# Optimization experiments

Hardware: AMD Instinct MI355X
Metric: run time of the kernel (lower is better)

## Reference

```python
import jax, jax.numpy as jnp
import numpy as np

OUT = 16          # output_size
SCALE = 1.0 / 16.0  # 1/featmap_stride
GRID = 2          # sampling_ratio


def setup_inputs() -> dict:
    key = jax.random.key(0)
    k1, k2, k3 = jax.random.split(key, 3)
    N, C, T, H, W, K = 2, 256, 16, 56, 56, 5
    feat = jax.random.normal(k1, (N, C, T, H, W), jnp.float32)
    img = H * 16.0  # 896 px input image
    xy = jax.random.uniform(k2, (N, K, 2), minval=0.0, maxval=img - 300.0)
    wh = jax.random.uniform(k3, (N, K, 2), minval=32.0, maxval=290.0)
    boxes = jnp.concatenate([xy, xy + wh], axis=-1)  # valid xyxy boxes
    rois = jnp.concatenate([jnp.zeros((N, K, 1)), boxes], axis=-1).astype(jnp.float32)
    entity_mask = jnp.ones((N, 1, K, T), dtype=bool)  # unused by forward (as in original)
    return {"feat": feat, "rois": rois, "entity_mask": entity_mask}


def _roi_align_single(feat_n, boxes):
    """RoIAlign (aligned=True, avg pool, fixed sampling grid) for one clip.

    feat_n: (C, T, H, W) -- applied to every frame t at once.
    boxes:  (K, 4) xyxy in input-image coordinates.
    returns (T, K, C, OUT, OUT)
    """
    C, T, H, W = feat_n.shape
    K = boxes.shape[0]
    b = boxes * SCALE - 0.5  # aligned=True offset
    x1, y1, x2, y2 = b[:, 0], b[:, 1], b[:, 2], b[:, 3]
    bin_w = (x2 - x1) / OUT
    bin_h = (y2 - y1) / OUT
    g = (jnp.arange(GRID, dtype=feat_n.dtype) + 0.5) / GRID
    p = jnp.arange(OUT, dtype=feat_n.dtype)
    # sample coords per roi/bin/grid-point: (K, OUT, GRID)
    xs = x1[:, None, None] + (p[None, :, None] + g[None, None, :]) * bin_w[:, None, None]
    ys = y1[:, None, None] + (p[None, :, None] + g[None, None, :]) * bin_h[:, None, None]
    # full (K, OUT_h, OUT_w, GRID_h, GRID_w) coordinate grids
    Y = jnp.broadcast_to(ys[:, :, None, :, None], (K, OUT, OUT, GRID, GRID))
    X = jnp.broadcast_to(xs[:, None, :, None, :], (K, OUT, OUT, GRID, GRID))
    valid = (Y > -1.0) & (Y < H) & (X > -1.0) & (X < W)
    Yc = jnp.clip(Y, 0.0, H - 1.0)
    Xc = jnp.clip(X, 0.0, W - 1.0)
    y0 = jnp.floor(Yc).astype(jnp.int32)
    x0 = jnp.floor(Xc).astype(jnp.int32)
    y1i = jnp.minimum(y0 + 1, H - 1)
    x1i = jnp.minimum(x0 + 1, W - 1)
    ly = Yc - y0.astype(feat_n.dtype)
    lx = Xc - x0.astype(feat_n.dtype)
    hy = 1.0 - ly
    hx = 1.0 - lx
    m = valid.astype(feat_n.dtype)
    gat = lambda yi, xi: feat_n[:, :, yi, xi]  # -> (C, T, K, OUT, OUT, GRID, GRID)
    val = (gat(y0, x0) * (hy * hx * m)
           + gat(y0, x1i) * (hy * lx * m)
           + gat(y1i, x0) * (ly * hx * m)
           + gat(y1i, x1i) * (ly * lx * m))
    out = val.mean(axis=(-1, -2))  # avg over GRIDxGRID samples (mmcv divides by count)
    return out.transpose(1, 2, 0, 3, 4)  # (T, K, C, OUT, OUT)


def reference(feat, rois, entity_mask):
    # feat: (N, C, T, H, W); rois: (N, K, 5); entity_mask unused (as in original forward)
    boxes = rois[..., 1:5]
    roi_feats = jax.vmap(_roi_align_single)(feat, boxes)  # (N, T, K, C, OUT, OUT)
    return roi_feats, feat
```

## Files before the change

kernel.cpp:

```cpp
#include <hip/hip_runtime.h>

constexpr int N = 2, C = 256, T = 16, H = 56, W = 56, K = 5, OUTP = 16;
constexpr int ROI_TOTAL  = N * T * K * C * OUTP * OUTP;
constexpr int FEAT_TOTAL = N * C * T * H * W;

__global__ __launch_bounds__(256) void roi_align_kernel(
    const float* __restrict__ feat,
    const float* __restrict__ rois,
    float* __restrict__ out)
{
    int idx = blockIdx.x * 256 + threadIdx.x;
    if (idx >= ROI_TOTAL) return;

    int px = idx & 15;
    int py = (idx >> 4) & 15;
    int c  = (idx >> 8) & 255;
    int rest = idx >> 16;
    int k  = rest % 5;
    int nt = rest / 5;
    int t  = nt & 15;
    int n  = nt >> 4;

    const float* r = rois + (n * K + k) * 5;
    float bx1 = r[1] * (1.0f / 16.0f) - 0.5f;
    float by1 = r[2] * (1.0f / 16.0f) - 0.5f;
    float bx2 = r[3] * (1.0f / 16.0f) - 0.5f;
    float by2 = r[4] * (1.0f / 16.0f) - 0.5f;
    float bw = (bx2 - bx1) * (1.0f / 16.0f);
    float bh = (by2 - by1) * (1.0f / 16.0f);

    const float* fp = feat + ((size_t)((n * C + c) * T + t)) * (H * W);

    float acc = 0.0f;
    #pragma unroll
    for (int gy = 0; gy < 2; ++gy) {
        float Yf = by1 + ((float)py + (gy ? 0.75f : 0.25f)) * bh;
        #pragma unroll
        for (int gx = 0; gx < 2; ++gx) {
            float Xf = bx1 + ((float)px + (gx ? 0.75f : 0.25f)) * bw;
            if (Yf > -1.0f && Yf < (float)H && Xf > -1.0f && Xf < (float)W) {
                float Yc = fminf(fmaxf(Yf, 0.0f), (float)(H - 1));
                float Xc = fminf(fmaxf(Xf, 0.0f), (float)(W - 1));
                int y0 = (int)Yc;
                int x0 = (int)Xc;
                int y1i = min(y0 + 1, H - 1);
                int x1i = min(x0 + 1, W - 1);
                float ly = Yc - (float)y0;
                float lx = Xc - (float)x0;
                float hy = 1.0f - ly;
                float hx = 1.0f - lx;
                const float* row0 = fp + y0  * W;
                const float* row1 = fp + y1i * W;
                acc += row0[x0]  * hy * hx
                     + row0[x1i] * hy * lx
                     + row1[x0]  * ly * hx
                     + row1[x1i] * ly * lx;
            }
        }
    }
    out[idx] = acc * 0.25f;
}

extern "C" void kernel_launch(void* const* d_in, const int* in_sizes, int n_in,
                              void* d_out, int out_size, void* d_ws, size_t ws_size,
                              hipStream_t stream)
{
    const float* feat = (const float*)d_in[0];
    const float* rois = (const float*)d_in[1];

    float* roi_out  = (float*)d_out;
    float* feat_out = (float*)d_out + ROI_TOTAL;

    hipMemcpyAsync(feat_out, feat, (size_t)FEAT_TOTAL * sizeof(float),
                   hipMemcpyDeviceToDevice, stream);

    roi_align_kernel<<<ROI_TOTAL / 256, 256, 0, stream>>>(feat, rois, roi_out);
}
```

Baseline: 263.0 us.

## Fuse feature passthrough copy into RoIAlign kernel and compute four outputs per thread

Replaces the separate device-to-device memcpy with copy blocks inside a single fused kernel, so the passthrough copy and the RoIAlign work share one launch and can overlap. Each RoIAlign thread now computes four adjacent x outputs, hoisting the y interpolation setup and writing a float4. This cuts launch and serialization overhead and improves store width, at the cost of fewer threads and more registers per thread.

Result: slower. 313.1 us (+19.0%).

```diff
diff --git a/kernel.cpp b/kernel.cpp
--- a/kernel.cpp
+++ b/kernel.cpp
@@ -1,21 +1,29 @@
 #include <hip/hip_runtime.h>
 
 constexpr int N = 2, C = 256, T = 16, H = 56, W = 56, K = 5, OUTP = 16;
-constexpr int ROI_TOTAL  = N * T * K * C * OUTP * OUTP;
-constexpr int FEAT_TOTAL = N * C * T * H * W;
+constexpr int ROI_TOTAL   = N * T * K * C * OUTP * OUTP;
+constexpr int FEAT_TOTAL  = N * C * T * H * W;
+constexpr int COPY_BLOCKS = FEAT_TOTAL / 4 / 256;
+constexpr int ROI_BLOCKS  = ROI_TOTAL / 4 / 256;
 
-__global__ __launch_bounds__(256) void roi_align_kernel(
+__global__ __launch_bounds__(256) void fused_roi_copy_kernel(
     const float* __restrict__ feat,
     const float* __restrict__ rois,
-    float* __restrict__ out)
+    float* __restrict__ roi_out,
+    float* __restrict__ feat_out)
 {
-    int idx = blockIdx.x * 256 + threadIdx.x;
-    if (idx >= ROI_TOTAL) return;
+    int b = blockIdx.x;
+    if (b < COPY_BLOCKS) {
+        int i = b * 256 + threadIdx.x;
+        ((float4*)feat_out)[i] = ((const float4*)feat)[i];
+        return;
+    }
 
-    int px = idx & 15;
-    int py = (idx >> 4) & 15;
-    int c  = (idx >> 8) & 255;
-    int rest = idx >> 16;
+    int rid = (b - COPY_BLOCKS) * 256 + threadIdx.x;
+    int px0  = (rid & 3) * 4;
+    int py   = (rid >> 2) & 15;
+    int c    = (rid >> 6) & 255;
+    int rest = rid >> 14;
     int k  = rest % 5;
     int nt = rest / 5;
     int t  = nt & 15;
@@ -31,34 +39,45 @@
 
     const float* fp = feat + ((size_t)((n * C + c) * T + t)) * (H * W);
 
-    float acc = 0.0f;
+    float res[4] = {0.f, 0.f, 0.f, 0.f};
+
     #pragma unroll
     for (int gy = 0; gy < 2; ++gy) {
         float Yf = by1 + ((float)py + (gy ? 0.75f : 0.25f)) * bh;
-        #pragma unroll
-        for (int gx = 0; gx < 2; ++gx) {
-            float Xf = bx1 + ((float)px + (gx ? 0.75f : 0.25f)) * bw;
-            if (Yf > -1.0f && Yf < (float)H && Xf > -1.0f && Xf < (float)W) {
-                float Yc = fminf(fmaxf(Yf, 0.0f), (float)(H - 1));
-                float Xc = fminf(fmaxf(Xf, 0.0f), (float)(W - 1));
-                int y0 = (int)Yc;
-                int x0 = (int)Xc;
-                int y1i = min(y0 + 1, H - 1);
-                int x1i = min(x0 + 1, W - 1);
-                float ly = Yc - (float)y0;
-                float lx = Xc - (float)x0;
-                float hy = 1.0f - ly;
-                float hx = 1.0f - lx;
-                const float* row0 = fp + y0  * W;
-                const float* row1 = fp + y1i * W;
-                acc += row0[x0]  * hy * hx
-                     + row0[x1i] * hy * lx
-                     + row1[x0]  * ly * hx
-                     + row1[x1i] * ly * lx;
+        if (Yf > -1.0f && Yf < (float)H) {
+            float Yc = fminf(fmaxf(Yf, 0.0f), (float)(H - 1));
+            int   y0  = (int)Yc;
+            int   y1i = min(y0 + 1, H - 1);
+            float ly  = Yc - (float)y0;
+            float hy  = 1.0f - ly;
+            const float* row0 = fp + y0  * W;
+            const float* row1 = fp + y1i * W;
+            #pragma unroll
+            for (int j = 0; j < 4; ++j) {
+                float pxf = (float)(px0 + j);
+                #pragma unroll
+                for (int gx = 0; gx < 2; ++gx) {
+                    float Xf = bx1 + (pxf + (gx ? 0.75f : 0.25f)) * bw;
+                    if (Xf > -1.0f && Xf < (float)W) {
+                        float Xc  = fminf(fmaxf(Xf, 0.0f), (float)(W - 1));
+                        int   x0  = (int)Xc;
+                        int   x1i = min(x0 + 1, W - 1);
+                        float lx  = Xc - (float)x0;
+                        float hx  = 1.0f - lx;
+                        res[j] += (row0[x0] * hx + row0[x1i] * lx) * hy
+                                + (row1[x0] * hx + row1[x1i] * lx) * ly;
+                    }
+                }
             }
         }
     }
-    out[idx] = acc * 0.25f;
+
+    float4 o;
+    o.x = res[0] * 0.25f;
+    o.y = res[1] * 0.25f;
+    o.z = res[2] * 0.25f;
+    o.w = res[3] * 0.25f;
+    ((float4*)roi_out)[rid] = o;
 }
 
 extern "C" void kernel_launch(void* const* d_in, const int* in_sizes, int n_in,
@@ -71,8 +90,6 @@
     float* roi_out  = (float*)d_out;
     float* feat_out = (float*)d_out + ROI_TOTAL;
 
-    hipMemcpyAsync(feat_out, feat, (size_t)FEAT_TOTAL * sizeof(float),
-                   hipMemcpyDeviceToDevice, stream);
-
-    roi_align_kernel<<<ROI_TOTAL / 256, 256, 0, stream>>>(feat, rois, roi_out);
+    fused_roi_copy_kernel<<<COPY_BLOCKS + ROI_BLOCKS, 256, 0, stream>>>(
+        feat, rois, roi_out, feat_out);
 }
```
